# Optimization experiments

Measured on AMD Instinct MI355X. Metric: run time of the kernel, lower is better.

Reference implementation:

```python
import jax, jax.numpy as jnp
import numpy as np

N = 100000   # nodes
E = 3200000  # edges (avg degree 32)
NFEAT = 512
NHID = 8     # forced == 8 by (x_left + x_right) broadcast in the source
NCLASS = 16


def setup_inputs() -> dict:
    key = jax.random.key(0)
    ks = jax.random.split(key, 10)
    x = jax.random.normal(ks[0], (N, NFEAT), dtype=jnp.float32)
    adj_rows = jax.random.randint(ks[1], (E,), 0, N, dtype=jnp.int32)
    adj_cols = jax.random.randint(ks[2], (E,), 0, N, dtype=jnp.int32)
    adj_vals = jax.random.uniform(ks[3], (E,), dtype=jnp.float32)
    s1 = 1.0 / np.sqrt(NFEAT)
    s2 = 1.0 / np.sqrt(NHID)
    W1 = jax.random.normal(ks[4], (NFEAT, NHID), dtype=jnp.float32) * s1
    b1 = jnp.zeros((NHID,), dtype=jnp.float32)
    W2 = jax.random.normal(ks[5], (NHID, NCLASS), dtype=jnp.float32) * s2
    b2 = jnp.zeros((NCLASS,), dtype=jnp.float32)
    V = jax.random.normal(ks[6], (NFEAT, NHID), dtype=jnp.float32) * s1
    gamma = jnp.ones((NHID,), dtype=jnp.float32)
    beta = jnp.zeros((NHID,), dtype=jnp.float32)
    return {"x": x, "adj_rows": adj_rows, "adj_cols": adj_cols, "adj_vals": adj_vals,
            "W1": W1, "b1": b1, "W2": W2, "b2": b2, "V": V, "gamma": gamma, "beta": beta}


def reference(x, adj_rows, adj_cols, adj_vals, W1, b1, W2, b2, V, gamma, beta):
    n = x.shape[0]

    def spmm(support):  # adj @ support, adj in COO
        gathered = adj_vals[:, None] * support[adj_cols]        # [E, F]
        return jax.ops.segment_sum(gathered, adj_rows, num_segments=n)

    # gc1: relu(spmm(adj, x @ W1) + b1)   (dropout off: eval mode)
    x_left = jax.nn.relu(spmm(x @ W1) + b1)                     # [N, 8]

    # BI_Intereaction: FM bi-interaction pooling 0.5*((xV)^2 - (x^2)(V^2))
    xv = x @ V                                                  # [N, 8]
    x2v2 = (x * x) @ (V * V)                                    # [N, 8]
    x_right = jax.nn.relu(0.5 * (xv * xv - x2v2))

    # BatchNorm1d eval mode: running_mean=0, running_var=1 -> affine only
    x_right = gamma * x_right + beta

    h = 0.5 * (x_left + x_right)                                # [N, 8]
    out = spmm(h @ W2) + b2                                     # [N, 16]
    return jax.nn.log_softmax(out, axis=1)
```

## Files before the change

### kernel.cpp

```cpp
#include <hip/hip_runtime.h>
#include <cstdint>
#include <cstddef>


#define NFEAT 512
#define NHID 8
#define NCLASS 16
#define RPB 128
#define NB 512
#define BCAP 4608

#define DB_NODES 64
#define DB_CHUNK 32
#define DB_PAD 33
#define DB_BUF (DB_NODES * DB_PAD)

__device__ __forceinline__ void dense_body2(
    int node0, int tid,
    const float* __restrict__ x,
    const float* __restrict__ W1T, const float* __restrict__ VT,
    const float* __restrict__ VSQT,
    const float* __restrict__ gamma, const float* __restrict__ beta,
    float* __restrict__ xw1, float* __restrict__ right, int n_nodes,
    float* xs)
{
    const int lane = tid & 63;

    const int j0 = __builtin_amdgcn_readfirstlane(tid >> 6);
    const float* __restrict__ w1a = W1T  + j0 * NFEAT;
    const float* __restrict__ w1b = W1T  + (j0 + 4) * NFEAT;
    const float* __restrict__ va  = VT   + j0 * NFEAT;
    const float* __restrict__ vb  = VT   + (j0 + 4) * NFEAT;
    const float* __restrict__ sa  = VSQT + j0 * NFEAT;
    const float* __restrict__ sb  = VSQT + (j0 + 4) * NFEAT;

    const int row0 = tid >> 3, row1 = row0 + 32;
    const int col  = tid & 7;
    int gr0 = node0 + row0; if (gr0 >= n_nodes) gr0 = n_nodes - 1;
    int gr1 = node0 + row1; if (gr1 >= n_nodes) gr1 = n_nodes - 1;
    const float4* __restrict__ p0 = (const float4*)(x + (size_t)gr0 * NFEAT) + col;
    const float4* __restrict__ p1 = (const float4*)(x + (size_t)gr1 * NFEAT) + col;
    const int b0 = row0 * DB_PAD + col * 4;
    const int b1 = row1 * DB_PAD + col * 4;

    float a1a = 0.f, a1b = 0.f;
    float ava = 0.f, avb = 0.f;
    float a2a = 0.f, a2b = 0.f;
    const int xbase = lane * DB_PAD;

    {
        float4 c0 = p0[0], c1 = p1[0];
        xs[b0] = c0.x; xs[b0 + 1] = c0.y; xs[b0 + 2] = c0.z; xs[b0 + 3] = c0.w;
        xs[b1] = c1.x; xs[b1 + 1] = c1.y; xs[b1 + 2] = c1.z; xs[b1 + 3] = c1.w;
    }
    __syncthreads();

    for (int ch = 0; ch < NFEAT / DB_CHUNK; ++ch) {
        float4 n0, n1;
        const bool more = (ch + 1) < (NFEAT / DB_CHUNK);
        if (more) { n0 = p0[(ch + 1) * 8]; n1 = p1[(ch + 1) * 8]; }

        const float* xb = xs + (ch & 1) * DB_BUF + xbase;
        const int kof = ch * DB_CHUNK;
#pragma unroll 2
        for (int kk = 0; kk < DB_CHUNK / 4; ++kk) {
            const int kb = kof + kk * 4;
            float x0 = xb[kk * 4 + 0];
            float x1 = xb[kk * 4 + 1];
            float x2 = xb[kk * 4 + 2];
            float x3 = xb[kk * 4 + 3];
            float q0 = x0 * x0, q1 = x1 * x1, q2 = x2 * x2, q3 = x3 * x3;

            a1a += x0 * w1a[kb] + x1 * w1a[kb + 1] + x2 * w1a[kb + 2] + x3 * w1a[kb + 3];
            a1b += x0 * w1b[kb] + x1 * w1b[kb + 1] + x2 * w1b[kb + 2] + x3 * w1b[kb + 3];
            ava += x0 * va[kb]  + x1 * va[kb + 1]  + x2 * va[kb + 2]  + x3 * va[kb + 3];
            avb += x0 * vb[kb]  + x1 * vb[kb + 1]  + x2 * vb[kb + 2]  + x3 * vb[kb + 3];
            a2a += q0 * sa[kb]  + q1 * sa[kb + 1]  + q2 * sa[kb + 2]  + q3 * sa[kb + 3];
            a2b += q0 * sb[kb]  + q1 * sb[kb + 1]  + q2 * sb[kb + 2]  + q3 * sb[kb + 3];
        }

        if (more) {
            float* d = xs + ((ch + 1) & 1) * DB_BUF;
            d[b0] = n0.x; d[b0 + 1] = n0.y; d[b0 + 2] = n0.z; d[b0 + 3] = n0.w;
            d[b1] = n1.x; d[b1 + 1] = n1.y; d[b1 + 2] = n1.z; d[b1 + 3] = n1.w;
        }
        __syncthreads();
    }

    int node = node0 + lane;
    if (node < n_nodes) {
        float g0 = gamma[j0], g1 = gamma[j0 + 4];
        float b0_ = beta[j0], b1_ = beta[j0 + 4];
        xw1[node * 8 + j0]     = a1a;
        xw1[node * 8 + j0 + 4] = a1b;
        float ra = fmaxf(0.5f * (ava * ava - a2a), 0.f);
        float rb = fmaxf(0.5f * (avb * avb - a2b), 0.f);
        right[node * 8 + j0]     = 0.5f * (g0 * ra + b0_);
        right[node * 8 + j0 + 4] = 0.5f * (g1 * rb + b1_);
    }
}

__global__ __launch_bounds__(256) void dense_kernel(
    const float* __restrict__ x,
    const float* __restrict__ W1T, const float* __restrict__ VT,
    const float* __restrict__ VSQT,
    const float* __restrict__ gamma, const float* __restrict__ beta,
    float* __restrict__ xw1, float* __restrict__ right, int n_nodes)
{
    __shared__ float xs[2 * DB_BUF];
    dense_body2(blockIdx.x * DB_NODES, threadIdx.x, x, W1T, VT, VSQT,
                gamma, beta, xw1, right, n_nodes, xs);
}

__global__ __launch_bounds__(256) void count_prep_kernel(
    const int* __restrict__ rows, int* __restrict__ hist,
    int chunk, int nbins, int e,
    const float* __restrict__ W1, const float* __restrict__ V,
    float* __restrict__ W1T, float* __restrict__ VT, float* __restrict__ VSQT)
{
    __shared__ int histl[2112];
    const int bid = blockIdx.x;
    const int tid = threadIdx.x;

    int gt = bid * 256 + tid;
    if (gt < NFEAT * NHID) {
        int k = gt >> 3, j = gt & 7;
        W1T[j * NFEAT + k] = W1[gt];
        float vv = V[gt];
        VT[j * NFEAT + k] = vv;
        VSQT[j * NFEAT + k] = vv * vv;
    }

    for (int i = tid; i < nbins; i += 256) histl[i] = 0;
    __syncthreads();

    const int base = bid * chunk;
    int lim = e - base; if (lim > chunk) lim = chunk; if (lim < 0) lim = 0;
    const int nq = lim >> 2;
    for (int q = tid; q < nq; q += 256) {
        int4 r4 = *(const int4*)(rows + base + q * 4);
        atomicAdd(&histl[r4.x >> 7], 1);
        atomicAdd(&histl[r4.y >> 7], 1);
        atomicAdd(&histl[r4.z >> 7], 1);
        atomicAdd(&histl[r4.w >> 7], 1);
    }
    const int rem = lim & 3;
    if (tid < rem) atomicAdd(&histl[rows[base + nq * 4 + tid] >> 7], 1);
    __syncthreads();
    for (int i = tid; i < nbins; i += 256)
        hist[(size_t)i * NB + bid] = histl[i];
}

__global__ __launch_bounds__(NB) void scan_kernel(
    const int* __restrict__ hist, int* __restrict__ off,
    int* __restrict__ bintotal)
{
    __shared__ int sa[NB], sb[NB];
    const int bin = blockIdx.x;
    const int tid = threadIdx.x;
    const size_t base = (size_t)bin * NB;

    int h0 = hist[base + tid];
    sa[tid] = h0;
    __syncthreads();
    int* s = sa; int* d = sb;
    for (int o = 1; o < NB; o <<= 1) {
        d[tid] = s[tid] + (tid >= o ? s[tid - o] : 0);
        __syncthreads();
        int* t = s; s = d; d = t;
    }
    off[base + tid] = s[tid] - h0;
    if (tid == NB - 1) bintotal[bin] = s[NB - 1];
}

__global__ __launch_bounds__(256) void place_dense_kernel(
    const int* __restrict__ rows, const int* __restrict__ cols,
    const float* __restrict__ vals, const int* __restrict__ off,
    unsigned long long* __restrict__ binbuf,
    int chunk, int nbins, int e,
    const float* __restrict__ x, const float* __restrict__ W1T,
    const float* __restrict__ VT, const float* __restrict__ VSQT,
    const float* __restrict__ gamma, const float* __restrict__ beta,
    float* __restrict__ xw1, float* __restrict__ right,
    int n_nodes, int dblocks)
{
    __shared__ float xs[2 * DB_BUF];
    const int bid = blockIdx.x;
    const int tid = threadIdx.x;

    if (bid >= NB) {
        int g = bid - NB;
        if (g < dblocks)
            dense_body2(g * DB_NODES, tid, x, W1T, VT, VSQT,
                        gamma, beta, xw1, right, n_nodes, xs);
        return;
    }

    int* cur = (int*)xs;
    const int cb = bid;
    for (int i = tid; i < nbins; i += 256)
        cur[i] = off[(size_t)i * NB + cb];
    __syncthreads();

    const int base = cb * chunk;
    int lim = e - base; if (lim > chunk) lim = chunk; if (lim < 0) lim = 0;
    const int nq = lim >> 2;
    for (int q = tid; q < nq; q += 256) {
        int i = base + q * 4;
        int4   r4 = *(const int4*)(rows + i);
        int4   c4 = *(const int4*)(cols + i);
        float4 v4 = *(const float4*)(vals + i);
#pragma unroll
        for (int u = 0; u < 4; ++u) {
            int r = (&r4.x)[u], c = (&c4.x)[u];
            float v = (&v4.x)[u];
            int bin = r >> 7;
            int slot = atomicAdd(&cur[bin], 1);
            if (slot < BCAP) {
                unsigned long long ev =
                    ((unsigned long long)__float_as_uint(v) << 32) |
                    ((unsigned)(r & (RPB - 1)) << 17) | (unsigned)(unsigned int)c;
                binbuf[(size_t)bin * BCAP + slot] = ev;
            }
        }
    }
    const int rem = lim & 3;
    if (tid < rem) {
        int i = base + nq * 4 + tid;
        int r = rows[i];
        int bin = r >> 7;
        int slot = atomicAdd(&cur[bin], 1);
        if (slot < BCAP) {
            unsigned long long ev =
                ((unsigned long long)__float_as_uint(vals[i]) << 32) |
                ((unsigned)(r & (RPB - 1)) << 17) | (unsigned)(unsigned int)cols[i];
            binbuf[(size_t)bin * BCAP + slot] = ev;
        }
    }
}

__global__ __launch_bounds__(512) void binspmm0_kernel(
    const unsigned long long* __restrict__ binbuf,
    const int* __restrict__ bintotal,
    unsigned long long* __restrict__ sortbuf,
    int* __restrict__ rowstart, int* __restrict__ rowcnt,
    const float* __restrict__ src,
    const float* __restrict__ b1, const float* __restrict__ right,
    float* __restrict__ dst, int n)
{
    __shared__ unsigned long long sorted[BCAP];
    __shared__ int hcnt[RPB];
    __shared__ int hstart[RPB];
    __shared__ int hcur[RPB];
    const int bin = blockIdx.x;
    const int tid = threadIdx.x;

    if (tid < RPB) hcnt[tid] = 0;
    __syncthreads();

    int total = bintotal[bin];
    if (total > BCAP) total = BCAP;
    const unsigned long long* bb = binbuf + (size_t)bin * BCAP;

    for (int s = tid; s < total; s += 512) {
        unsigned long long ev = bb[s];
        atomicAdd(&hcnt[(int)((ev >> 17) & (RPB - 1))], 1);
    }
    __syncthreads();

    if (tid < RPB) hstart[tid] = hcnt[tid];
    __syncthreads();
    for (int o = 1; o < RPB; o <<= 1) {
        int t = 0;
        if (tid < RPB) t = hstart[tid] + (tid >= o ? hstart[tid - o] : 0);
        __syncthreads();
        if (tid < RPB) hstart[tid] = t;
        __syncthreads();
    }
    if (tid < RPB) {
        int ex = hstart[tid] - hcnt[tid];
        hstart[tid] = ex;
        hcur[tid] = ex;
    }
    __syncthreads();

    for (int s = tid; s < total; s += 512) {
        unsigned long long ev = bb[s];
        int rl = (int)((ev >> 17) & (RPB - 1));
        int slot = atomicAdd(&hcur[rl], 1);
        sorted[slot] = ev;
    }
    __syncthreads();

    for (int s = tid; s < total; s += 512)
        sortbuf[(size_t)bin * BCAP + s] = sorted[s];
    if (tid < RPB) {
        rowstart[bin * RPB + tid] = hstart[tid];
        rowcnt[bin * RPB + tid]   = hcnt[tid];
    }

    const int rl = tid >> 2, l = tid & 3;
    const int st = hstart[rl], cn = hcnt[rl];
    float a0 = 0.f, a1 = 0.f, a2 = 0.f, a3 = 0.f;
    float a4 = 0.f, a5 = 0.f, a6 = 0.f, a7 = 0.f;
    for (int i = st + l; i < st + cn; i += 4) {
        unsigned long long ev = sorted[i];
        int col = (int)(ev & 0x1FFFFu);
        float v = __uint_as_float((unsigned)(ev >> 32));
        const float4* sp = (const float4*)(src + (size_t)col * 8);
        float4 lo = sp[0], hi = sp[1];
        a0 += v * lo.x; a1 += v * lo.y; a2 += v * lo.z; a3 += v * lo.w;
        a4 += v * hi.x; a5 += v * hi.y; a6 += v * hi.z; a7 += v * hi.w;
    }
#pragma unroll
    for (int off2 = 1; off2 < 4; off2 <<= 1) {
        a0 += __shfl_xor(a0, off2); a1 += __shfl_xor(a1, off2);
        a2 += __shfl_xor(a2, off2); a3 += __shfl_xor(a3, off2);
        a4 += __shfl_xor(a4, off2); a5 += __shfl_xor(a5, off2);
        a6 += __shfl_xor(a6, off2); a7 += __shfl_xor(a7, off2);
    }

    const int g = bin * RPB + rl;
    if (g >= n) return;

    float s0, s1;
    if (l == 0)      { s0 = a0; s1 = a1; }
    else if (l == 1) { s0 = a2; s1 = a3; }
    else if (l == 2) { s0 = a4; s1 = a5; }
    else             { s0 = a6; s1 = a7; }
    float2 bb2 = ((const float2*)b1)[l];
    float2 rv  = *(const float2*)(right + (size_t)g * 8 + l * 2);
    float2 w;
    w.x = 0.5f * fmaxf(s0 + bb2.x, 0.f) + rv.x;
    w.y = 0.5f * fmaxf(s1 + bb2.y, 0.f) + rv.y;
    *(float2*)(dst + (size_t)g * 8 + l * 2) = w;
}

__global__ __launch_bounds__(512) void walk1_kernel(
    const unsigned long long* __restrict__ sortbuf,
    const int* __restrict__ rowstart, const int* __restrict__ rowcnt,
    const float* __restrict__ src,
    const float* __restrict__ W2, const float* __restrict__ b2,
    float* __restrict__ out, int n)
{
    const int bin = blockIdx.x;
    const int tid = threadIdx.x;
    const int rl = tid >> 2, l = tid & 3;

    const int st = rowstart[bin * RPB + rl];
    const int cn = rowcnt[bin * RPB + rl];
    const unsigned long long* bb = sortbuf + (size_t)bin * BCAP;

    float a0 = 0.f, a1 = 0.f, a2 = 0.f, a3 = 0.f;
    float a4 = 0.f, a5 = 0.f, a6 = 0.f, a7 = 0.f;
    for (int i = st + l; i < st + cn; i += 4) {
        unsigned long long ev = bb[i];
        int col = (int)(ev & 0x1FFFFu);
        float v = __uint_as_float((unsigned)(ev >> 32));
        const float4* sp = (const float4*)(src + (size_t)col * 8);
        float4 lo = sp[0], hi = sp[1];
        a0 += v * lo.x; a1 += v * lo.y; a2 += v * lo.z; a3 += v * lo.w;
        a4 += v * hi.x; a5 += v * hi.y; a6 += v * hi.z; a7 += v * hi.w;
    }
#pragma unroll
    for (int off2 = 1; off2 < 4; off2 <<= 1) {
        a0 += __shfl_xor(a0, off2); a1 += __shfl_xor(a1, off2);
        a2 += __shfl_xor(a2, off2); a3 += __shfl_xor(a3, off2);
        a4 += __shfl_xor(a4, off2); a5 += __shfl_xor(a5, off2);
        a6 += __shfl_xor(a6, off2); a7 += __shfl_xor(a7, off2);
    }

    const int g = bin * RPB + rl;
    if (g >= n) return;

    float hv[NHID] = {a0, a1, a2, a3, a4, a5, a6, a7};
    float z[NCLASS];
#pragma unroll
    for (int cc = 0; cc < NCLASS; ++cc) z[cc] = b2[cc];
#pragma unroll
    for (int j = 0; j < NHID; ++j) {
#pragma unroll
        for (int cc = 0; cc < NCLASS; ++cc)
            z[cc] += hv[j] * W2[j * NCLASS + cc];
    }
    float m = z[0];
#pragma unroll
    for (int cc = 1; cc < NCLASS; ++cc) m = fmaxf(m, z[cc]);
    float s = 0.f;
#pragma unroll
    for (int cc = 0; cc < NCLASS; ++cc) s += __expf(z[cc] - m);
    float lse = m + __logf(s);
    float o0 = z[4 * l + 0] - lse;
    float o1 = z[4 * l + 1] - lse;
    float o2 = z[4 * l + 2] - lse;
    float o3 = z[4 * l + 3] - lse;
    *(float4*)(out + (size_t)g * NCLASS + 4 * l) = make_float4(o0, o1, o2, o3);
}

__global__ __launch_bounds__(256) void prep_kernel(
    const float* __restrict__ W1, const float* __restrict__ V,
    float* __restrict__ W1T, float* __restrict__ VT, float* __restrict__ VSQT,
    uint4* __restrict__ zero_base, int zero_count16)
{
    int tid = blockIdx.x * 256 + threadIdx.x;
    if (tid < NFEAT * NHID) {
        int k = tid >> 3, j = tid & 7;
        W1T[j * NFEAT + k] = W1[tid];
        float vv = V[tid];
        VT[j * NFEAT + k] = vv;
        VSQT[j * NFEAT + k] = vv * vv;
    }
    int stride = gridDim.x * 256;
    for (int i = tid; i < zero_count16; i += stride)
        zero_base[i] = make_uint4(0u, 0u, 0u, 0u);
}

__global__ __launch_bounds__(256) void spmm8_kernel(
    const int* __restrict__ rows, const int* __restrict__ cols,
    const float* __restrict__ vals, const float* __restrict__ src,
    float* __restrict__ acc, int n_edges)
{
    int tid = blockIdx.x * 256 + threadIdx.x;
    int e = tid >> 1;
    if (e >= n_edges) return;
    int hh = tid & 1;
    int r = rows[e], c = cols[e];
    float v = vals[e];
    float4 f = ((const float4*)src)[c * 2 + hh];
    float* d = acc + (size_t)r * NHID + hh * 4;
    unsafeAtomicAdd(d + 0, v * f.x);
    unsafeAtomicAdd(d + 1, v * f.y);
    unsafeAtomicAdd(d + 2, v * f.z);
    unsafeAtomicAdd(d + 3, v * f.w);
}

__global__ __launch_bounds__(256) void mid_kernel(
    const float* __restrict__ acc1, const float* __restrict__ right,
    const float* __restrict__ b1, float* __restrict__ h, int n4)
{
    int i = blockIdx.x * 256 + threadIdx.x;
    if (i >= n4) return;
    float4 a = ((const float4*)acc1)[i];
    float4 r = ((const float4*)right)[i];
    float4 b = ((const float4*)b1)[i & 1];
    float4 o;
    o.x = 0.5f * fmaxf(a.x + b.x, 0.f) + r.x;
    o.y = 0.5f * fmaxf(a.y + b.y, 0.f) + r.y;
    o.z = 0.5f * fmaxf(a.z + b.z, 0.f) + r.z;
    o.w = 0.5f * fmaxf(a.w + b.w, 0.f) + r.w;
    ((float4*)h)[i] = o;
}

__global__ __launch_bounds__(256) void final_kernel(
    const float* __restrict__ acc2, const float* __restrict__ W2,
    const float* __restrict__ b2, float* __restrict__ out, int n_nodes)
{
    int node = blockIdx.x * 256 + threadIdx.x;
    if (node >= n_nodes) return;
    float4 h0 = ((const float4*)acc2)[(size_t)node * 2];
    float4 h1 = ((const float4*)acc2)[(size_t)node * 2 + 1];
    float hv[NHID] = {h0.x, h0.y, h0.z, h0.w, h1.x, h1.y, h1.z, h1.w};
    float z[NCLASS];
#pragma unroll
    for (int c = 0; c < NCLASS; ++c) z[c] = b2[c];
#pragma unroll
    for (int j = 0; j < NHID; ++j) {
#pragma unroll
        for (int c = 0; c < NCLASS; ++c) z[c] += hv[j] * W2[j * NCLASS + c];
    }
    float m = z[0];
#pragma unroll
    for (int c = 1; c < NCLASS; ++c) m = fmaxf(m, z[c]);
    float s = 0.f;
#pragma unroll
    for (int c = 0; c < NCLASS; ++c) s += __expf(z[c] - m);
    float l = m + __logf(s);
    float4* o = (float4*)(out + (size_t)node * NCLASS);
#pragma unroll
    for (int q = 0; q < 4; ++q) {
        float4 tq;
        tq.x = z[4 * q + 0] - l;
        tq.y = z[4 * q + 1] - l;
        tq.z = z[4 * q + 2] - l;
        tq.w = z[4 * q + 3] - l;
        o[q] = tq;
    }
}

extern "C" void kernel_launch(void* const* d_in, const int* in_sizes, int n_in,
                              void* d_out, int out_size, void* d_ws, size_t ws_size,
                              hipStream_t stream)
{
    const float* x     = (const float*)d_in[0];
    const int*   rows  = (const int*)  d_in[1];
    const int*   cols  = (const int*)  d_in[2];
    const float* vals  = (const float*)d_in[3];
    const float* W1    = (const float*)d_in[4];
    const float* b1    = (const float*)d_in[5];
    const float* W2    = (const float*)d_in[6];
    const float* b2    = (const float*)d_in[7];
    const float* V     = (const float*)d_in[8];
    const float* gamma = (const float*)d_in[9];
    const float* beta  = (const float*)d_in[10];

    const int n = in_sizes[0] / NFEAT;
    const int e = in_sizes[1];
    const int nbins = (n + RPB - 1) / RPB;
    const int dblocks = (n + DB_NODES - 1) / DB_NODES;

    float* ws = (float*)d_ws;

    float* xw1   = ws;
    float* right = ws + (size_t)n * 8;
    float* h     = ws + (size_t)n * 16;
    float* W1T   = ws + (size_t)n * 24;
    float* VT    = W1T + NFEAT * NHID;
    float* VSQT  = VT + NFEAT * NHID;
    const size_t fixedf = (size_t)n * 24 + 3 * NFEAT * NHID;
    int* hist     = (int*)(ws + fixedf);
    int* off      = hist + (size_t)nbins * NB;
    int* bintotal = off + (size_t)nbins * NB;
    int* rowstart = bintotal + nbins;
    int* rowcnt   = rowstart + (size_t)nbins * RPB;
    size_t bb_off = (fixedf + 2ull * nbins * NB + nbins + 2ull * nbins * RPB + 1)
                    & ~(size_t)1;
    unsigned long long* binbuf  = (unsigned long long*)(ws + bb_off);
    unsigned long long* sortbuf = binbuf + (size_t)nbins * BCAP;

    const size_t needf = bb_off + 4ull * nbins * BCAP;
    const bool use_fast =
        (n <= (1 << 17)) && (nbins <= 2112) && (needf * 4 <= ws_size);

    if (use_fast) {
        int chunk = ((e + NB - 1) / NB + 3) & ~3;

        count_prep_kernel<<<NB, 256, 0, stream>>>(
            rows, hist, chunk, nbins, e, W1, V, W1T, VT, VSQT);

        scan_kernel<<<nbins, NB, 0, stream>>>(hist, off, bintotal);

        place_dense_kernel<<<NB + dblocks, 256, 0, stream>>>(
            rows, cols, vals, off, binbuf, chunk, nbins, e,
            x, W1T, VT, VSQT, gamma, beta, xw1, right, n, dblocks);

        binspmm0_kernel<<<nbins, 512, 0, stream>>>(
            binbuf, bintotal, sortbuf, rowstart, rowcnt,
            xw1, b1, right, h, n);

        walk1_kernel<<<nbins, 512, 0, stream>>>(
            sortbuf, rowstart, rowcnt, h, W2, b2, (float*)d_out, n);
    } else {
        float* f_acc1  = ws;
        float* f_acc2  = ws + (size_t)n * 8;
        float* f_xw1   = ws + (size_t)n * 16;
        float* f_right = ws + (size_t)n * 24;
        float* f_h     = ws + (size_t)n * 32;
        float* f_W1T   = ws + (size_t)n * 40;
        float* f_VT    = f_W1T + NFEAT * NHID;
        float* f_VSQT  = f_VT + NFEAT * NHID;

        prep_kernel<<<(n * 4 + 255) / 256, 256, 0, stream>>>(
            W1, V, f_W1T, f_VT, f_VSQT, (uint4*)ws, n * 4);

        dense_kernel<<<dblocks, 256, 0, stream>>>(
            x, f_W1T, f_VT, f_VSQT, gamma, beta, f_xw1, f_right, n);

        spmm8_kernel<<<(e * 2 + 255) / 256, 256, 0, stream>>>(rows, cols, vals, f_xw1, f_acc1, e);
        mid_kernel<<<(n * 2 + 255) / 256, 256, 0, stream>>>(f_acc1, f_right, b1, f_h, n * 2);
        spmm8_kernel<<<(e * 2 + 255) / 256, 256, 0, stream>>>(rows, cols, vals, f_h, f_acc2, e);
        final_kernel<<<(n + 255) / 256, 256, 0, stream>>>(f_acc2, W2, b2, (float*)d_out, n);
    }
}
```

Before: 448.2 us.

## Halve row bins, split dense GEMV across count and place kernels

Row bins shrink from 128 to 64 rows, so there are twice as many bins with smaller capacity. The aggregation now uses 8 lanes per row and keeps bin entries in registers across the counting and scatter passes instead of reloading them. Half of the dense x@W/V projection blocks now run inside the histogram kernel and the other half inside the placement kernel, and weight transposition moves to a small separate prep kernel. The aim is to balance the two launches and overlap compute-bound dense work with memory-bound edge binning, at the cost of an extra launch. Two smaller changes are a fully unrolled inner dense loop and a 256-thread walk kernel.

Result: no change. 457.0 us (+2.0%).

```diff
diff --git a/kernel.cpp b/kernel.cpp
--- a/kernel.cpp
+++ b/kernel.cpp
@@ -6,9 +6,10 @@
 #define NFEAT 512
 #define NHID 8
 #define NCLASS 16
-#define RPB 128
+#define RPB 64
 #define NB 512
-#define BCAP 4608
+#define BCAP 2368
+#define NBINS_MAX 2048
 
 #define DB_NODES 64
 #define DB_CHUNK 32
@@ -62,7 +63,7 @@
 
         const float* xb = xs + (ch & 1) * DB_BUF + xbase;
         const int kof = ch * DB_CHUNK;
-#pragma unroll 2
+#pragma unroll
         for (int kk = 0; kk < DB_CHUNK / 4; ++kk) {
             const int kb = kof + kk * 4;
             float x0 = xb[kk * 4 + 0];
@@ -112,43 +113,63 @@
                 gamma, beta, xw1, right, n_nodes, xs);
 }
 
-__global__ __launch_bounds__(256) void count_prep_kernel(
+__global__ __launch_bounds__(256) void prep_kernel(
+    const float* __restrict__ W1, const float* __restrict__ V,
+    float* __restrict__ W1T, float* __restrict__ VT, float* __restrict__ VSQT,
+    uint4* __restrict__ zero_base, int zero_count16)
+{
+    int tid = blockIdx.x * 256 + threadIdx.x;
+    if (tid < NFEAT * NHID) {
+        int k = tid >> 3, j = tid & 7;
+        W1T[j * NFEAT + k] = W1[tid];
+        float vv = V[tid];
+        VT[j * NFEAT + k] = vv;
+        VSQT[j * NFEAT + k] = vv * vv;
+    }
+    int stride = gridDim.x * 256;
+    for (int i = tid; i < zero_count16; i += stride)
+        zero_base[i] = make_uint4(0u, 0u, 0u, 0u);
+}
+
+__global__ __launch_bounds__(256) void count_denseA_kernel(
     const int* __restrict__ rows, int* __restrict__ hist,
     int chunk, int nbins, int e,
-    const float* __restrict__ W1, const float* __restrict__ V,
-    float* __restrict__ W1T, float* __restrict__ VT, float* __restrict__ VSQT)
-{
-    __shared__ int histl[2112];
+    const float* __restrict__ x, const float* __restrict__ W1T,
+    const float* __restrict__ VT, const float* __restrict__ VSQT,
+    const float* __restrict__ gamma, const float* __restrict__ beta,
+    float* __restrict__ xw1, float* __restrict__ right,
+    int n_nodes, int dblocksA)
+{
+    __shared__ float xs[2 * DB_BUF];
     const int bid = blockIdx.x;
     const int tid = threadIdx.x;
 
-    int gt = bid * 256 + tid;
-    if (gt < NFEAT * NHID) {
-        int k = gt >> 3, j = gt & 7;
-        W1T[j * NFEAT + k] = W1[gt];
-        float vv = V[gt];
-        VT[j * NFEAT + k] = vv;
-        VSQT[j * NFEAT + k] = vv * vv;
-    }
-
+    if (bid < dblocksA) {
+        dense_body2(bid * DB_NODES, tid, x, W1T, VT, VSQT,
+                    gamma, beta, xw1, right, n_nodes, xs);
+        return;
+    }
+
+    const int cb = bid - dblocksA;
+    int* histl = (int*)xs;
     for (int i = tid; i < nbins; i += 256) histl[i] = 0;
     __syncthreads();
 
-    const int base = bid * chunk;
+    const int base = cb * chunk;
     int lim = e - base; if (lim > chunk) lim = chunk; if (lim < 0) lim = 0;
     const int nq = lim >> 2;
     for (int q = tid; q < nq; q += 256) {
         int4 r4 = *(const int4*)(rows + base + q * 4);
-        atomicAdd(&histl[r4.x >> 7], 1);
-        atomicAdd(&histl[r4.y >> 7], 1);
-        atomicAdd(&histl[r4.z >> 7], 1);
-        atomicAdd(&histl[r4.w >> 7], 1);
+        atomicAdd(&histl[r4.x >> 6], 1);
+        atomicAdd(&histl[r4.y >> 6], 1);
+        atomicAdd(&histl[r4.z >> 6], 1);
+        atomicAdd(&histl[r4.w >> 6], 1);
     }
     const int rem = lim & 3;
-    if (tid < rem) atomicAdd(&histl[rows[base + nq * 4 + tid] >> 7], 1);
+    if (tid < rem) atomicAdd(&histl[rows[base + nq * 4 + tid] >> 6], 1);
     __syncthreads();
     for (int i = tid; i < nbins; i += 256)
-        hist[(size_t)i * NB + bid] = histl[i];
+        hist[(size_t)i * NB + cb] = histl[i];
 }
 
 __global__ __launch_bounds__(NB) void scan_kernel(
@@ -173,7 +194,7 @@
     if (tid == NB - 1) bintotal[bin] = s[NB - 1];
 }
 
-__global__ __launch_bounds__(256) void place_dense_kernel(
+__global__ __launch_bounds__(256) void place_denseB_kernel(
     const int* __restrict__ rows, const int* __restrict__ cols,
     const float* __restrict__ vals, const int* __restrict__ off,
     unsigned long long* __restrict__ binbuf,
@@ -182,22 +203,20 @@
     const float* __restrict__ VT, const float* __restrict__ VSQT,
     const float* __restrict__ gamma, const float* __restrict__ beta,
     float* __restrict__ xw1, float* __restrict__ right,
-    int n_nodes, int dblocks)
+    int n_nodes, int dblocksB, int nodeB0)
 {
     __shared__ float xs[2 * DB_BUF];
     const int bid = blockIdx.x;
     const int tid = threadIdx.x;
 
-    if (bid >= NB) {
-        int g = bid - NB;
-        if (g < dblocks)
-            dense_body2(g * DB_NODES, tid, x, W1T, VT, VSQT,
-                        gamma, beta, xw1, right, n_nodes, xs);
+    if (bid < dblocksB) {
+        dense_body2(nodeB0 + bid * DB_NODES, tid, x, W1T, VT, VSQT,
+                    gamma, beta, xw1, right, n_nodes, xs);
         return;
     }
 
+    const int cb = bid - dblocksB;
     int* cur = (int*)xs;
-    const int cb = bid;
     for (int i = tid; i < nbins; i += 256)
         cur[i] = off[(size_t)i * NB + cb];
     __syncthreads();
@@ -214,7 +233,7 @@
         for (int u = 0; u < 4; ++u) {
             int r = (&r4.x)[u], c = (&c4.x)[u];
             float v = (&v4.x)[u];
-            int bin = r >> 7;
+            int bin = r >> 6;
             int slot = atomicAdd(&cur[bin], 1);
             if (slot < BCAP) {
                 unsigned long long ev =
@@ -228,7 +247,7 @@
     if (tid < rem) {
         int i = base + nq * 4 + tid;
         int r = rows[i];
-        int bin = r >> 7;
+        int bin = r >> 6;
         int slot = atomicAdd(&cur[bin], 1);
         if (slot < BCAP) {
             unsigned long long ev =
@@ -262,10 +281,13 @@
     if (total > BCAP) total = BCAP;
     const unsigned long long* bb = binbuf + (size_t)bin * BCAP;
 
-    for (int s = tid; s < total; s += 512) {
-        unsigned long long ev = bb[s];
-        atomicAdd(&hcnt[(int)((ev >> 17) & (RPB - 1))], 1);
-    }
+    const int s0 = tid, s1 = tid + 512, s2 = tid + 1024, s3 = tid + 1536, s4 = tid + 2048;
+    unsigned long long e0 = 0, e1 = 0, e2 = 0, e3 = 0, e4 = 0;
+    if (s0 < total) { e0 = bb[s0]; atomicAdd(&hcnt[(int)((e0 >> 17) & (RPB - 1))], 1); }
+    if (s1 < total) { e1 = bb[s1]; atomicAdd(&hcnt[(int)((e1 >> 17) & (RPB - 1))], 1); }
+    if (s2 < total) { e2 = bb[s2]; atomicAdd(&hcnt[(int)((e2 >> 17) & (RPB - 1))], 1); }
+    if (s3 < total) { e3 = bb[s3]; atomicAdd(&hcnt[(int)((e3 >> 17) & (RPB - 1))], 1); }
+    if (s4 < total) { e4 = bb[s4]; atomicAdd(&hcnt[(int)((e4 >> 17) & (RPB - 1))], 1); }
     __syncthreads();
 
     if (tid < RPB) hstart[tid] = hcnt[tid];
@@ -284,12 +306,11 @@
     }
     __syncthreads();
 
-    for (int s = tid; s < total; s += 512) {
-        unsigned long long ev = bb[s];
-        int rl = (int)((ev >> 17) & (RPB - 1));
-        int slot = atomicAdd(&hcur[rl], 1);
-        sorted[slot] = ev;
-    }
+    if (s0 < total) { int rl = (int)((e0 >> 17) & (RPB - 1)); sorted[atomicAdd(&hcur[rl], 1)] = e0; }
+    if (s1 < total) { int rl = (int)((e1 >> 17) & (RPB - 1)); sorted[atomicAdd(&hcur[rl], 1)] = e1; }
+    if (s2 < total) { int rl = (int)((e2 >> 17) & (RPB - 1)); sorted[atomicAdd(&hcur[rl], 1)] = e2; }
+    if (s3 < total) { int rl = (int)((e3 >> 17) & (RPB - 1)); sorted[atomicAdd(&hcur[rl], 1)] = e3; }
+    if (s4 < total) { int rl = (int)((e4 >> 17) & (RPB - 1)); sorted[atomicAdd(&hcur[rl], 1)] = e4; }
     __syncthreads();
 
     for (int s = tid; s < total; s += 512)
@@ -299,11 +320,11 @@
         rowcnt[bin * RPB + tid]   = hcnt[tid];
     }
 
-    const int rl = tid >> 2, l = tid & 3;
+    const int rl = tid >> 3, l = tid & 7;
     const int st = hstart[rl], cn = hcnt[rl];
     float a0 = 0.f, a1 = 0.f, a2 = 0.f, a3 = 0.f;
     float a4 = 0.f, a5 = 0.f, a6 = 0.f, a7 = 0.f;
-    for (int i = st + l; i < st + cn; i += 4) {
+    for (int i = st + l; i < st + cn; i += 8) {
         unsigned long long ev = sorted[i];
         int col = (int)(ev & 0x1FFFFu);
         float v = __uint_as_float((unsigned)(ev >> 32));
@@ -313,30 +334,23 @@
         a4 += v * hi.x; a5 += v * hi.y; a6 += v * hi.z; a7 += v * hi.w;
     }
 #pragma unroll
-    for (int off2 = 1; off2 < 4; off2 <<= 1) {
-        a0 += __shfl_xor(a0, off2); a1 += __shfl_xor(a1, off2);
-        a2 += __shfl_xor(a2, off2); a3 += __shfl_xor(a3, off2);
-        a4 += __shfl_xor(a4, off2); a5 += __shfl_xor(a5, off2);
-        a6 += __shfl_xor(a6, off2); a7 += __shfl_xor(a7, off2);
+    for (int o2 = 1; o2 < 8; o2 <<= 1) {
+        a0 += __shfl_xor(a0, o2); a1 += __shfl_xor(a1, o2);
+        a2 += __shfl_xor(a2, o2); a3 += __shfl_xor(a3, o2);
+        a4 += __shfl_xor(a4, o2); a5 += __shfl_xor(a5, o2);
+        a6 += __shfl_xor(a6, o2); a7 += __shfl_xor(a7, o2);
     }
 
     const int g = bin * RPB + rl;
     if (g >= n) return;
 
-    float s0, s1;
-    if (l == 0)      { s0 = a0; s1 = a1; }
-    else if (l == 1) { s0 = a2; s1 = a3; }
-    else if (l == 2) { s0 = a4; s1 = a5; }
-    else             { s0 = a6; s1 = a7; }
-    float2 bb2 = ((const float2*)b1)[l];
-    float2 rv  = *(const float2*)(right + (size_t)g * 8 + l * 2);
-    float2 w;
-    w.x = 0.5f * fmaxf(s0 + bb2.x, 0.f) + rv.x;
-    w.y = 0.5f * fmaxf(s1 + bb2.y, 0.f) + rv.y;
-    *(float2*)(dst + (size_t)g * 8 + l * 2) = w;
-}
-
-__global__ __launch_bounds__(512) void walk1_kernel(
+    float s = l < 4 ? (l < 2 ? (l == 0 ? a0 : a1) : (l == 2 ? a2 : a3))
+                    : (l < 6 ? (l == 4 ? a4 : a5) : (l == 6 ? a6 : a7));
+    float hv = 0.5f * fmaxf(s + b1[l], 0.f) + right[(size_t)g * 8 + l];
+    dst[(size_t)g * 8 + l] = hv;
+}
+
+__global__ __launch_bounds__(256) void walk1_kernel(
     const unsigned long long* __restrict__ sortbuf,
     const int* __restrict__ rowstart, const int* __restrict__ rowcnt,
     const float* __restrict__ src,
@@ -363,11 +377,11 @@
         a4 += v * hi.x; a5 += v * hi.y; a6 += v * hi.z; a7 += v * hi.w;
     }
 #pragma unroll
-    for (int off2 = 1; off2 < 4; off2 <<= 1) {
-        a0 += __shfl_xor(a0, off2); a1 += __shfl_xor(a1, off2);
-        a2 += __shfl_xor(a2, off2); a3 += __shfl_xor(a3, off2);
-        a4 += __shfl_xor(a4, off2); a5 += __shfl_xor(a5, off2);
-        a6 += __shfl_xor(a6, off2); a7 += __shfl_xor(a7, off2);
+    for (int o2 = 1; o2 < 4; o2 <<= 1) {
+        a0 += __shfl_xor(a0, o2); a1 += __shfl_xor(a1, o2);
+        a2 += __shfl_xor(a2, o2); a3 += __shfl_xor(a3, o2);
+        a4 += __shfl_xor(a4, o2); a5 += __shfl_xor(a5, o2);
+        a6 += __shfl_xor(a6, o2); a7 += __shfl_xor(a7, o2);
     }
 
     const int g = bin * RPB + rl;
@@ -390,29 +404,13 @@
 #pragma unroll
     for (int cc = 0; cc < NCLASS; ++cc) s += __expf(z[cc] - m);
     float lse = m + __logf(s);
-    float o0 = z[4 * l + 0] - lse;
-    float o1 = z[4 * l + 1] - lse;
-    float o2 = z[4 * l + 2] - lse;
-    float o3 = z[4 * l + 3] - lse;
-    *(float4*)(out + (size_t)g * NCLASS + 4 * l) = make_float4(o0, o1, o2, o3);
-}
-
-__global__ __launch_bounds__(256) void prep_kernel(
-    const float* __restrict__ W1, const float* __restrict__ V,
-    float* __restrict__ W1T, float* __restrict__ VT, float* __restrict__ VSQT,
-    uint4* __restrict__ zero_base, int zero_count16)
-{
-    int tid = blockIdx.x * 256 + threadIdx.x;
-    if (tid < NFEAT * NHID) {
-        int k = tid >> 3, j = tid & 7;
-        W1T[j * NFEAT + k] = W1[tid];
-        float vv = V[tid];
-        VT[j * NFEAT + k] = vv;
-        VSQT[j * NFEAT + k] = vv * vv;
-    }
-    int stride = gridDim.x * 256;
-    for (int i = tid; i < zero_count16; i += stride)
-        zero_base[i] = make_uint4(0u, 0u, 0u, 0u);
+    float o0, o1, o2, o3;
+    if (l == 0)      { o0 = z[0];  o1 = z[1];  o2 = z[2];  o3 = z[3];  }
+    else if (l == 1) { o0 = z[4];  o1 = z[5];  o2 = z[6];  o3 = z[7];  }
+    else if (l == 2) { o0 = z[8];  o1 = z[9];  o2 = z[10]; o3 = z[11]; }
+    else             { o0 = z[12]; o1 = z[13]; o2 = z[14]; o3 = z[15]; }
+    *(float4*)(out + (size_t)g * NCLASS + 4 * l) =
+        make_float4(o0 - lse, o1 - lse, o2 - lse, o3 - lse);
 }
 
 __global__ __launch_bounds__(256) void spmm8_kernel(
@@ -507,6 +505,9 @@
     const int e = in_sizes[1];
     const int nbins = (n + RPB - 1) / RPB;
     const int dblocks = (n + DB_NODES - 1) / DB_NODES;
+    const int dblocksA = dblocks / 2;
+    const int nodeB0 = dblocksA * DB_NODES;
+    const int dblocksB = dblocks - dblocksA;
 
     float* ws = (float*)d_ws;
 
@@ -529,25 +530,29 @@
 
     const size_t needf = bb_off + 4ull * nbins * BCAP;
     const bool use_fast =
-        (n <= (1 << 17)) && (nbins <= 2112) && (needf * 4 <= ws_size);
+        (n <= (1 << 17)) && (nbins <= NBINS_MAX) && (needf * 4 <= ws_size);
 
     if (use_fast) {
         int chunk = ((e + NB - 1) / NB + 3) & ~3;
 
-        count_prep_kernel<<<NB, 256, 0, stream>>>(
-            rows, hist, chunk, nbins, e, W1, V, W1T, VT, VSQT);
+        prep_kernel<<<16, 256, 0, stream>>>(
+            W1, V, W1T, VT, VSQT, (uint4*)ws, 0);
+
+        count_denseA_kernel<<<dblocksA + NB, 256, 0, stream>>>(
+            rows, hist, chunk, nbins, e,
+            x, W1T, VT, VSQT, gamma, beta, xw1, right, n, dblocksA);
 
         scan_kernel<<<nbins, NB, 0, stream>>>(hist, off, bintotal);
 
-        place_dense_kernel<<<NB + dblocks, 256, 0, stream>>>(
+        place_denseB_kernel<<<dblocksB + NB, 256, 0, stream>>>(
             rows, cols, vals, off, binbuf, chunk, nbins, e,
-            x, W1T, VT, VSQT, gamma, beta, xw1, right, n, dblocks);
+            x, W1T, VT, VSQT, gamma, beta, xw1, right, n, dblocksB, nodeB0);
 
         binspmm0_kernel<<<nbins, 512, 0, stream>>>(
             binbuf, bintotal, sortbuf, rowstart, rowcnt,
             xw1, b1, right, h, n);
 
-        walk1_kernel<<<nbins, 512, 0, stream>>>(
+        walk1_kernel<<<nbins, 256, 0, stream>>>(
             sortbuf, rowstart, rowcnt, h, W2, b2, (float*)d_out, n);
     } else {
         float* f_acc1  = ws;
```
